# Performance work log

Hardware: AMD Instinct MI355X
Metric: run time of the kernel (lower is better)

## Reference

```python
import jax, jax.numpy as jnp
import numpy as np

B, N, C = 2, 2048, 1024
H = 16
HD = C // H  # 64


def setup_inputs() -> dict:
    key = jax.random.key(0)
    k1, k2, k3 = jax.random.split(key, 3)
    x = jax.random.normal(k1, (B, N, C), dtype=jnp.float32)
    w_qkv = jax.random.normal(k2, (C, 3 * C), dtype=jnp.float32) * (C ** -0.5)
    b_qkv = jnp.zeros((3 * C,), dtype=jnp.float32)
    w_out = jax.random.normal(k3, (C, C), dtype=jnp.float32) * (C ** -0.5)
    b_out = jnp.zeros((C,), dtype=jnp.float32)
    return {"x": x, "w_qkv": w_qkv, "b_qkv": b_qkv, "w_out": w_out, "b_out": b_out}


def reference(x, w_qkv, b_qkv, w_out, b_out):
    scale = HD ** -0.5
    # QKV projection: (B,N,3C) -> (B,N,3,H,HD) -> (B,3,H,N,HD)
    qkv = (jnp.einsum('bnc,cd->bnd', x, w_qkv) + b_qkv)
    qkv = qkv.reshape(B, N, 3, H, HD).transpose(0, 2, 3, 1, 4)
    q, k, v = qkv[:, 0], qkv[:, 1], qkv[:, 2]  # each (B,H,N,HD)
    # scaled dot-product attention with full NxN matrix (as in source)
    attn = jnp.einsum('bhnd,bhmd->bhnm', q, k) * scale
    attn = jax.nn.softmax(attn, axis=-1)
    out = jnp.einsum('bhnm,bhmd->bhnd', attn, v)  # (B,H,N,HD)
    out = out.transpose(0, 2, 1, 3).reshape(B, N, C)
    out = jnp.einsum('bnc,cd->bnd', out, w_out) + b_out
    return out
```

## Files before the change

kernel.cpp:

```cpp
#include <hip/hip_runtime.h>
#include <stdint.h>

using uint = unsigned int;
using ushort = unsigned short;

constexpr int Bb = 2;
constexpr int Ns = 2048;
constexpr int Cd = 1024;
constexpr int Hh = 16;
constexpr int HD = 64;
constexpr int BHND = Bb * Hh * Ns * HD;

constexpr float QSCL = 0.18033688f;

typedef __attribute__((ext_vector_type(8))) short short8;
typedef __attribute__((ext_vector_type(4))) float floatx4;

__device__ inline ushort f2bf(float f) {
  uint u = __float_as_uint(f);
  return (ushort)((u + 0x7fffu + ((u >> 16) & 1u)) >> 16);
}
__device__ inline ushort f2bfr(float f) {
  return (ushort)((__float_as_uint(f) + 0x8000u) >> 16);
}
__device__ inline uint cvt_pk_bf16(float lo, float hi) {
  uint r;
  asm("v_cvt_pk_bf16_f32 %0, %1, %2" : "=v"(r) : "v"(lo), "v"(hi));
  return r;
}

__global__ __launch_bounds__(256) void cvt_f32_bf16(
    const float* __restrict__ in, ushort* __restrict__ outp) {
  const int i = blockIdx.x * 256 + threadIdx.x;
  const float4 v = ((const float4*)in)[i];
  ushort4 o;
  o.x = f2bf(v.x); o.y = f2bf(v.y); o.z = f2bf(v.z); o.w = f2bf(v.w);
  ((ushort4*)outp)[i] = o;
}

__global__ __launch_bounds__(256) void transpose_f32_bf16(
    const float* __restrict__ in, ushort* __restrict__ outp, int R, int Cc) {
  __shared__ alignas(16) ushort tile[32][33];
  const int c0 = blockIdx.x * 32, r0 = blockIdx.y * 32;
  const int tx = threadIdx.x & 31;
  const int ty = threadIdx.x >> 5;
#pragma unroll
  for (int i = 0; i < 4; ++i)
    tile[ty + 8 * i][tx] = f2bf(in[(size_t)(r0 + ty + 8 * i) * Cc + c0 + tx]);
  __syncthreads();
#pragma unroll
  for (int i = 0; i < 4; ++i)
    outp[(size_t)(c0 + ty + 8 * i) * R + r0 + tx] = tile[tx][ty + 8 * i];
}

template <int MODE>
__global__ __launch_bounds__(256) void gemm_bt(
    const ushort* __restrict__ A, const ushort* __restrict__ Bt,
    const float* __restrict__ bias, void* __restrict__ outp,
    int M, int K, int Nn) {
  constexpr int LDT = 40;
  __shared__ alignas(16) ushort As[128 * LDT];
  __shared__ alignas(16) ushort Bs[128 * LDT];
  const int tid = threadIdx.x;
  const int wave = tid >> 6, lane = tid & 63;
  const int quad = lane >> 4, l16 = lane & 15;
  const int wr = wave >> 1, wc = wave & 1;
  const int m0 = blockIdx.x * 128, n0 = blockIdx.y * 128;

  const int srow0 = tid >> 2;
  const int skc = (tid & 3) * 8;

  const ushort* pa = A + (size_t)(m0 + srow0) * K + skc;
  const ushort* pb = Bt + (size_t)(n0 + srow0) * K + skc;

  floatx4 acc[4][4];
#pragma unroll
  for (int i = 0; i < 4; ++i)
#pragma unroll
    for (int j = 0; j < 4; ++j) {
      acc[i][j][0] = 0.f; acc[i][j][1] = 0.f; acc[i][j][2] = 0.f; acc[i][j][3] = 0.f;
    }

  uint4 ra0 = *(const uint4*)(pa);
  uint4 ra1 = *(const uint4*)(pa + (size_t)64 * K);
  uint4 rb0 = *(const uint4*)(pb);
  uint4 rb1 = *(const uint4*)(pb + (size_t)64 * K);

  const int nkt = K >> 5;
  for (int kt = 0; kt < nkt; ++kt) {
    __syncthreads();
    *(uint4*)&As[srow0 * LDT + skc] = ra0;
    *(uint4*)&As[(srow0 + 64) * LDT + skc] = ra1;
    *(uint4*)&Bs[srow0 * LDT + skc] = rb0;
    *(uint4*)&Bs[(srow0 + 64) * LDT + skc] = rb1;
    __syncthreads();
    if (kt + 1 < nkt) {
      const ushort* qa = pa + (size_t)(kt + 1) * 32;
      const ushort* qb = pb + (size_t)(kt + 1) * 32;
      ra0 = *(const uint4*)(qa);
      ra1 = *(const uint4*)(qa + (size_t)64 * K);
      rb0 = *(const uint4*)(qb);
      rb1 = *(const uint4*)(qb + (size_t)64 * K);
    }
    short8 af[4], bfv[4];
#pragma unroll
    for (int mt = 0; mt < 4; ++mt)
      af[mt] = *(const short8*)&As[(wr * 64 + mt * 16 + l16) * LDT + quad * 8];
#pragma unroll
    for (int nt = 0; nt < 4; ++nt)
      bfv[nt] = *(const short8*)&Bs[(wc * 64 + nt * 16 + l16) * LDT + quad * 8];
#pragma unroll
    for (int mt = 0; mt < 4; ++mt)
#pragma unroll
      for (int nt = 0; nt < 4; ++nt)
        acc[mt][nt] = __builtin_amdgcn_mfma_f32_16x16x32_bf16(af[mt], bfv[nt],
                                                              acc[mt][nt], 0, 0, 0);
  }

  if (MODE == 0) {
    ushort* qp = (ushort*)outp;
    ushort* kp = qp + BHND;
    ushort* vp = qp + 2 * BHND;
#pragma unroll
    for (int nt = 0; nt < 4; ++nt) {
      const int gn = n0 + wc * 64 + nt * 16 + l16;
      const float bv = bias[gn];
      const int which = gn >> 10, cc = gn & 1023;
      const int h = cc >> 6, d = cc & 63;
      const float sc = (which == 0) ? QSCL : 1.0f;
#pragma unroll
      for (int mt = 0; mt < 4; ++mt) {
#pragma unroll
        for (int r = 0; r < 4; ++r) {
          const int gm = m0 + wr * 64 + mt * 16 + quad * 4 + r;
          const int b = gm >> 11, n = gm & 2047;
          const ushort o = f2bfr((acc[mt][nt][r] + bv) * sc);
          const int bh = b * Hh + h;
          if (which == 0)
            qp[((size_t)bh * Ns + n) * HD + d] = o;
          else if (which == 1)
            kp[((size_t)bh * Ns + n) * HD + d] = o;
          else
            vp[((size_t)bh * HD + d) * Ns + n] = o;
        }
      }
    }
  } else {
    float* fout = (float*)outp;
#pragma unroll
    for (int nt = 0; nt < 4; ++nt) {
      const int gn = n0 + wc * 64 + nt * 16 + l16;
      const float bv = bias[gn];
#pragma unroll
      for (int mt = 0; mt < 4; ++mt)
#pragma unroll
        for (int r = 0; r < 4; ++r) {
          const int gm = m0 + wr * 64 + mt * 16 + quad * 4 + r;
          fout[(size_t)gm * Nn + gn] = acc[mt][nt][r] + bv;
        }
    }
  }
}

__global__ __launch_bounds__(256, 2) void attn(
    const ushort* __restrict__ q, const ushort* __restrict__ k,
    const ushort* __restrict__ vT, ushort* __restrict__ aout) {
  constexpr int LDK = 72;
  __shared__ alignas(16) ushort Ks[64 * LDK];
  __shared__ alignas(16) ushort Vs[64 * LDK];
  const int tid = threadIdx.x;
  const int wave = tid >> 6, lane = tid & 63;
  const int quad = lane >> 4, l16 = lane & 15;
  const int bh = blockIdx.y;
  const int qw = blockIdx.x * 128 + wave * 32;

  const ushort* kb = k + (size_t)bh * Ns * HD;
  const ushort* vb = vT + (size_t)bh * HD * Ns;

  short8 aq[2][2];
#pragma unroll
  for (int nqi = 0; nqi < 2; ++nqi) {
    const ushort* qp = q + ((size_t)bh * Ns + qw + nqi * 16 + l16) * HD + quad * 8;
    aq[nqi][0] = *(const short8*)(qp);
    aq[nqi][1] = *(const short8*)(qp + 32);
  }

  floatx4 accO[4][2];
#pragma unroll
  for (int mt = 0; mt < 4; ++mt)
#pragma unroll
    for (int nqi = 0; nqi < 2; ++nqi) {
      accO[mt][nqi][0] = 0.f; accO[mt][nqi][1] = 0.f;
      accO[mt][nqi][2] = 0.f; accO[mt][nqi][3] = 0.f;
    }
  float lst[2] = {0.f, 0.f};
  const floatx4 fz = {0.f, 0.f, 0.f, 0.f};

  const int srow = tid >> 2;
  const int g0 = (tid & 3) * 2;
  const int cbA = (g0 >> 2) * 8 + ((g0 >> 1) & 1);
  const int g1 = g0 + 1;
  const int cbB = (g1 >> 2) * 8 + 4 + ((g1 >> 1) & 1);

  const ushort* kgp = kb + (size_t)srow * HD + g0 * 8;
  const ushort* vgp = vb + (size_t)srow * Ns + g0 * 8;
  ushort* ksw = &Ks[srow * LDK + g0 * 8];
  ushort* vswA = &Vs[srow * LDK + cbA * 4];
  ushort* vswB = &Vs[srow * LDK + cbB * 4];

  uint4 kg0 = *(const uint4*)(kgp);
  uint4 kg1 = *(const uint4*)(kgp + 8);
  uint4 vg0 = *(const uint4*)(vgp);
  uint4 vg1 = *(const uint4*)(vgp + 8);
  const ushort* kpre = kgp + 64 * HD;
  const ushort* vpre = vgp + 64;

  for (int kv0 = 0; kv0 < Ns; kv0 += 64) {
    __syncthreads();
    *(uint4*)ksw = kg0;
    *(uint4*)(ksw + 8) = kg1;
    *(uint2*)vswA = make_uint2(vg0.x, vg0.y);
    *(uint2*)(vswA + 8) = make_uint2(vg0.z, vg0.w);
    *(uint2*)vswB = make_uint2(vg1.x, vg1.y);
    *(uint2*)(vswB + 8) = make_uint2(vg1.z, vg1.w);
    __syncthreads();

    short8 ak[4][2], av[4][2];
#pragma unroll
    for (int t4 = 0; t4 < 4; ++t4) {
      const int ro = (t4 * 16 + l16) * LDK + quad * 8;
      ak[t4][0] = *(const short8*)&Ks[ro];
      ak[t4][1] = *(const short8*)&Ks[ro + 32];
      av[t4][0] = *(const short8*)&Vs[ro];
      av[t4][1] = *(const short8*)&Vs[ro + 32];
    }
    if (kv0 + 64 < Ns) {
      kg0 = *(const uint4*)(kpre);
      kg1 = *(const uint4*)(kpre + 8);
      vg0 = *(const uint4*)(vpre);
      vg1 = *(const uint4*)(vpre + 8);
      kpre += 64 * HD;
      vpre += 64;
    }

#pragma unroll
    for (int nqi = 0; nqi < 2; ++nqi) {
      floatx4 sacc[4];
      __builtin_amdgcn_s_setprio(1);
#pragma unroll
      for (int kvt = 0; kvt < 4; ++kvt)
        sacc[kvt] = __builtin_amdgcn_mfma_f32_16x16x32_bf16(
            ak[kvt][0], aq[nqi][0], fz, 0, 0, 0);
#pragma unroll
      for (int kvt = 0; kvt < 4; ++kvt)
        sacc[kvt] = __builtin_amdgcn_mfma_f32_16x16x32_bf16(
            ak[kvt][1], aq[nqi][1], sacc[kvt], 0, 0, 0);
      __builtin_amdgcn_s_setprio(0);

      uint pk[4][2];
      float ls = 0.f;
#pragma unroll
      for (int kvt = 0; kvt < 4; ++kvt) {
        const float p0 = __builtin_amdgcn_exp2f(sacc[kvt][0]);
        const float p1 = __builtin_amdgcn_exp2f(sacc[kvt][1]);
        const float p2 = __builtin_amdgcn_exp2f(sacc[kvt][2]);
        const float p3 = __builtin_amdgcn_exp2f(sacc[kvt][3]);
        ls += (p0 + p1) + (p2 + p3);
        pk[kvt][0] = cvt_pk_bf16(p0, p1);
        pk[kvt][1] = cvt_pk_bf16(p2, p3);
      }
      lst[nqi] += ls;

      __builtin_amdgcn_s_setprio(1);
#pragma unroll
      for (int ks = 0; ks < 2; ++ks) {
        union { uint u[4]; short8 s; } pf;
        pf.u[0] = pk[2 * ks][0]; pf.u[1] = pk[2 * ks][1];
        pf.u[2] = pk[2 * ks + 1][0]; pf.u[3] = pk[2 * ks + 1][1];
#pragma unroll
        for (int mt = 0; mt < 4; ++mt)
          accO[mt][nqi] = __builtin_amdgcn_mfma_f32_16x16x32_bf16(
              av[mt][ks], pf.s, accO[mt][nqi], 0, 0, 0);
      }
      __builtin_amdgcn_s_setprio(0);
    }
  }

  const int b = bh >> 4, h = bh & 15;
#pragma unroll
  for (int nqi = 0; nqi < 2; ++nqi) {
    float l = lst[nqi];
    l += __shfl_xor(l, 16, 64);
    l += __shfl_xor(l, 32, 64);
    const float inv = 1.f / l;
    const int n = qw + nqi * 16 + l16;
#pragma unroll
    for (int mt = 0; mt < 4; ++mt) {
      ushort4 o;
      o.x = f2bfr(accO[mt][nqi][0] * inv);
      o.y = f2bfr(accO[mt][nqi][1] * inv);
      o.z = f2bfr(accO[mt][nqi][2] * inv);
      o.w = f2bfr(accO[mt][nqi][3] * inv);
      *(ushort4*)&aout[((size_t)(b * Ns + n)) * Cd + h * HD + mt * 16 + quad * 4] = o;
    }
  }
}

extern "C" void kernel_launch(void* const* d_in, const int* in_sizes, int n_in,
                              void* d_out, int out_size, void* d_ws, size_t ws_size,
                              hipStream_t stream) {
  (void)in_sizes; (void)n_in; (void)out_size; (void)ws_size;
  const float* x = (const float*)d_in[0];
  const float* w_qkv = (const float*)d_in[1];
  const float* b_qkv = (const float*)d_in[2];
  const float* w_out = (const float*)d_in[3];
  const float* b_out = (const float*)d_in[4];

  ushort* xbf = (ushort*)d_ws;
  ushort* wqkvT = xbf + (size_t)BHND;
  ushort* woutT = wqkvT + 3072 * 1024;
  ushort* qkvbuf = woutT + 1024 * 1024;
  ushort* aout = qkvbuf + 3 * (size_t)BHND;

  cvt_f32_bf16<<<dim3(BHND / 1024), 256, 0, stream>>>(x, xbf);
  transpose_f32_bf16<<<dim3(96, 32), 256, 0, stream>>>(w_qkv, wqkvT, 1024, 3072);
  transpose_f32_bf16<<<dim3(32, 32), 256, 0, stream>>>(w_out, woutT, 1024, 1024);

  gemm_bt<0><<<dim3(32, 24), 256, 0, stream>>>(xbf, wqkvT, b_qkv, qkvbuf,
                                               4096, 1024, 3072);
  attn<<<dim3(16, 32), 256, 0, stream>>>(qkvbuf, qkvbuf + BHND,
                                         qkvbuf + 2 * (size_t)BHND, aout);
  gemm_bt<1><<<dim3(32, 8), 256, 0, stream>>>(aout, woutT, b_out, d_out,
                                              4096, 1024, 1024);
}
```

Before: 188.0 us.

## Double GEMM K-tile to 64 and remap workgroups across XCDs

Result: slower. 315.9 us (+68.1%).

```diff
diff --git a/kernel.cpp b/kernel.cpp
--- a/kernel.cpp
+++ b/kernel.cpp
@@ -58,20 +58,25 @@
     const ushort* __restrict__ A, const ushort* __restrict__ Bt,
     const float* __restrict__ bias, void* __restrict__ outp,
     int M, int K, int Nn) {
-  constexpr int LDT = 40;
+  constexpr int LDT = 72;
   __shared__ alignas(16) ushort As[128 * LDT];
   __shared__ alignas(16) ushort Bs[128 * LDT];
   const int tid = threadIdx.x;
   const int wave = tid >> 6, lane = tid & 63;
   const int quad = lane >> 4, l16 = lane & 15;
   const int wr = wave >> 1, wc = wave & 1;
-  const int m0 = blockIdx.x * 128, n0 = blockIdx.y * 128;
-
-  const int srow0 = tid >> 2;
-  const int skc = (tid & 3) * 8;
-
-  const ushort* pa = A + (size_t)(m0 + srow0) * K + skc;
-  const ushort* pb = Bt + (size_t)(n0 + srow0) * K + skc;
+
+  const int nwg = gridDim.x * gridDim.y;
+  int bid = blockIdx.x + gridDim.x * blockIdx.y;
+  bid = (bid & 7) * (nwg >> 3) + (bid >> 3);
+  const int m0 = (bid % gridDim.x) * 128;
+  const int n0 = (bid / gridDim.x) * 128;
+
+  const int srow = tid >> 3;
+  const int skc = (tid & 7) * 8;
+
+  const ushort* pa = A + (size_t)(m0 + srow) * K + skc;
+  const ushort* pb = Bt + (size_t)(n0 + srow) * K + skc;
 
   floatx4 acc[4][4];
 #pragma unroll
@@ -81,40 +86,52 @@
       acc[i][j][0] = 0.f; acc[i][j][1] = 0.f; acc[i][j][2] = 0.f; acc[i][j][3] = 0.f;
     }
 
-  uint4 ra0 = *(const uint4*)(pa);
-  uint4 ra1 = *(const uint4*)(pa + (size_t)64 * K);
-  uint4 rb0 = *(const uint4*)(pb);
-  uint4 rb1 = *(const uint4*)(pb + (size_t)64 * K);
-
-  const int nkt = K >> 5;
+  uint4 ra[4], rb[4];
+#pragma unroll
+  for (int c = 0; c < 4; ++c) {
+    ra[c] = *(const uint4*)(pa + (size_t)(32 * c) * K);
+    rb[c] = *(const uint4*)(pb + (size_t)(32 * c) * K);
+  }
+
+  const int nkt = K >> 6;
   for (int kt = 0; kt < nkt; ++kt) {
     __syncthreads();
-    *(uint4*)&As[srow0 * LDT + skc] = ra0;
-    *(uint4*)&As[(srow0 + 64) * LDT + skc] = ra1;
-    *(uint4*)&Bs[srow0 * LDT + skc] = rb0;
-    *(uint4*)&Bs[(srow0 + 64) * LDT + skc] = rb1;
+#pragma unroll
+    for (int c = 0; c < 4; ++c) {
+      *(uint4*)&As[(srow + 32 * c) * LDT + skc] = ra[c];
+      *(uint4*)&Bs[(srow + 32 * c) * LDT + skc] = rb[c];
+    }
     __syncthreads();
     if (kt + 1 < nkt) {
-      const ushort* qa = pa + (size_t)(kt + 1) * 32;
-      const ushort* qb = pb + (size_t)(kt + 1) * 32;
-      ra0 = *(const uint4*)(qa);
-      ra1 = *(const uint4*)(qa + (size_t)64 * K);
-      rb0 = *(const uint4*)(qb);
-      rb1 = *(const uint4*)(qb + (size_t)64 * K);
-    }
-    short8 af[4], bfv[4];
-#pragma unroll
-    for (int mt = 0; mt < 4; ++mt)
-      af[mt] = *(const short8*)&As[(wr * 64 + mt * 16 + l16) * LDT + quad * 8];
-#pragma unroll
-    for (int nt = 0; nt < 4; ++nt)
-      bfv[nt] = *(const short8*)&Bs[(wc * 64 + nt * 16 + l16) * LDT + quad * 8];
-#pragma unroll
-    for (int mt = 0; mt < 4; ++mt)
-#pragma unroll
-      for (int nt = 0; nt < 4; ++nt)
-        acc[mt][nt] = __builtin_amdgcn_mfma_f32_16x16x32_bf16(af[mt], bfv[nt],
-                                                              acc[mt][nt], 0, 0, 0);
+      const ushort* qa = pa + (size_t)(kt + 1) * 64;
+      const ushort* qb = pb + (size_t)(kt + 1) * 64;
+#pragma unroll
+      for (int c = 0; c < 4; ++c) {
+        ra[c] = *(const uint4*)(qa + (size_t)(32 * c) * K);
+        rb[c] = *(const uint4*)(qb + (size_t)(32 * c) * K);
+      }
+    }
+    short8 af[2][4], bfv[2][4];
+#pragma unroll
+    for (int mt = 0; mt < 4; ++mt) {
+      const int ro = (wr * 64 + mt * 16 + l16) * LDT + quad * 8;
+      af[0][mt] = *(const short8*)&As[ro];
+      af[1][mt] = *(const short8*)&As[ro + 32];
+    }
+#pragma unroll
+    for (int nt = 0; nt < 4; ++nt) {
+      const int ro = (wc * 64 + nt * 16 + l16) * LDT + quad * 8;
+      bfv[0][nt] = *(const short8*)&Bs[ro];
+      bfv[1][nt] = *(const short8*)&Bs[ro + 32];
+    }
+#pragma unroll
+    for (int kk = 0; kk < 2; ++kk)
+#pragma unroll
+      for (int mt = 0; mt < 4; ++mt)
+#pragma unroll
+        for (int nt = 0; nt < 4; ++nt)
+          acc[mt][nt] = __builtin_amdgcn_mfma_f32_16x16x32_bf16(
+              af[kk][mt], bfv[kk][nt], acc[mt][nt], 0, 0, 0);
   }
 
   if (MODE == 0) {
```

## Load GEMM tiles directly into LDS with global_load_lds

Applied to the files above, without the earlier changes.

New measurement: 197.1 us. +4.8%, slower.

```diff
diff --git a/kernel.cpp b/kernel.cpp
--- a/kernel.cpp
+++ b/kernel.cpp
@@ -27,6 +27,11 @@
   uint r;
   asm("v_cvt_pk_bf16_f32 %0, %1, %2" : "=v"(r) : "v"(lo), "v"(hi));
   return r;
+}
+__device__ inline void gld_lds16(const ushort* g, ushort* l) {
+  __builtin_amdgcn_global_load_lds(
+      (const __attribute__((address_space(1))) uint*)g,
+      (__attribute__((address_space(3))) uint*)l, 16, 0, 0);
 }
 
 __global__ __launch_bounds__(256) void cvt_f32_bf16(
@@ -58,20 +63,20 @@
     const ushort* __restrict__ A, const ushort* __restrict__ Bt,
     const float* __restrict__ bias, void* __restrict__ outp,
     int M, int K, int Nn) {
-  constexpr int LDT = 40;
-  __shared__ alignas(16) ushort As[128 * LDT];
-  __shared__ alignas(16) ushort Bs[128 * LDT];
+  __shared__ alignas(16) ushort As[128 * 32];
+  __shared__ alignas(16) ushort Bs[128 * 32];
   const int tid = threadIdx.x;
   const int wave = tid >> 6, lane = tid & 63;
   const int quad = lane >> 4, l16 = lane & 15;
   const int wr = wave >> 1, wc = wave & 1;
   const int m0 = blockIdx.x * 128, n0 = blockIdx.y * 128;
 
-  const int srow0 = tid >> 2;
-  const int skc = (tid & 3) * 8;
-
-  const ushort* pa = A + (size_t)(m0 + srow0) * K + skc;
-  const ushort* pb = Bt + (size_t)(n0 + srow0) * K + skc;
+  const int lrow = lane >> 2;
+  const int lgr = lane & 3;
+  const ushort* pa = A + (size_t)(m0 + wave * 32 + lrow) * K + lgr * 8;
+  const ushort* pb = Bt + (size_t)(n0 + wave * 32 + lrow) * K + lgr * 8;
+  ushort* lA = &As[wave * 32 * 32];
+  ushort* lB = &Bs[wave * 32 * 32];
 
   floatx4 acc[4][4];
 #pragma unroll
@@ -80,35 +85,25 @@
     for (int j = 0; j < 4; ++j) {
       acc[i][j][0] = 0.f; acc[i][j][1] = 0.f; acc[i][j][2] = 0.f; acc[i][j][3] = 0.f;
     }
-
-  uint4 ra0 = *(const uint4*)(pa);
-  uint4 ra1 = *(const uint4*)(pa + (size_t)64 * K);
-  uint4 rb0 = *(const uint4*)(pb);
-  uint4 rb1 = *(const uint4*)(pb + (size_t)64 * K);
 
   const int nkt = K >> 5;
   for (int kt = 0; kt < nkt; ++kt) {
     __syncthreads();
-    *(uint4*)&As[srow0 * LDT + skc] = ra0;
-    *(uint4*)&As[(srow0 + 64) * LDT + skc] = ra1;
-    *(uint4*)&Bs[srow0 * LDT + skc] = rb0;
-    *(uint4*)&Bs[(srow0 + 64) * LDT + skc] = rb1;
+    const ushort* qa = pa + kt * 32;
+    const ushort* qb = pb + kt * 32;
+    gld_lds16(qa, lA);
+    gld_lds16(qa + (size_t)16 * K, lA + 16 * 32);
+    gld_lds16(qb, lB);
+    gld_lds16(qb + (size_t)16 * K, lB + 16 * 32);
     __syncthreads();
-    if (kt + 1 < nkt) {
-      const ushort* qa = pa + (size_t)(kt + 1) * 32;
-      const ushort* qb = pb + (size_t)(kt + 1) * 32;
-      ra0 = *(const uint4*)(qa);
-      ra1 = *(const uint4*)(qa + (size_t)64 * K);
-      rb0 = *(const uint4*)(qb);
-      rb1 = *(const uint4*)(qb + (size_t)64 * K);
-    }
+
     short8 af[4], bfv[4];
 #pragma unroll
     for (int mt = 0; mt < 4; ++mt)
-      af[mt] = *(const short8*)&As[(wr * 64 + mt * 16 + l16) * LDT + quad * 8];
+      af[mt] = *(const short8*)&As[(wr * 64 + mt * 16 + l16) * 32 + quad * 8];
 #pragma unroll
     for (int nt = 0; nt < 4; ++nt)
-      bfv[nt] = *(const short8*)&Bs[(wc * 64 + nt * 16 + l16) * LDT + quad * 8];
+      bfv[nt] = *(const short8*)&Bs[(wc * 64 + nt * 16 + l16) * 32 + quad * 8];
 #pragma unroll
     for (int mt = 0; mt < 4; ++mt)
 #pragma unroll
```
